# Kernel tuning notes

Measured on AMD Instinct MI355X. Metric: run time of the kernel, lower is better.

The kernel has to match this reference:

```python
import jax, jax.numpy as jnp
import numpy as np

B, S, IN = 16, 512, 32
D, H, L = 768, 12, 6
DH = D // H
DFF = 4 * D
EPS = 1e-5
NEG = -1e9


def _ln(x, g, b):
    m = jnp.mean(x, axis=-1, keepdims=True)
    v = jnp.mean(jnp.square(x - m), axis=-1, keepdims=True)
    return (x - m) * jax.lax.rsqrt(v + EPS) * g + b


def setup_inputs() -> dict:
    key = jax.random.key(0)
    ks = jax.random.split(key, 24)
    nrm = lambda k, shape, s=0.02: jax.random.normal(k, shape, jnp.float32) * s
    inp = {
        'x': jax.random.normal(ks[0], (B, S, IN), jnp.float32),
        'event_lengths': jax.random.randint(ks[1], (B,), 1, S + 1),
        'in_w': nrm(ks[2], (IN, D)),
        'in_b': jnp.zeros((D,), jnp.float32),
        'pos_emb': nrm(ks[3], (S, D)),
        'qw': nrm(ks[4], (L, D, D)), 'qb': jnp.zeros((L, D), jnp.float32),
        'kw': nrm(ks[5], (L, D, D)), 'kb': jnp.zeros((L, D), jnp.float32),
        'vw': nrm(ks[6], (L, D, D)), 'vb': jnp.zeros((L, D), jnp.float32),
        'w1': nrm(ks[7], (L, D, DFF)), 'b1': jnp.zeros((L, DFF), jnp.float32),
        'w2': nrm(ks[8], (L, DFF, D)), 'b2': jnp.zeros((L, D), jnp.float32),
        'ln1_g': jnp.ones((L, D), jnp.float32), 'ln1_b': jnp.zeros((L, D), jnp.float32),
        'ln2_g': jnp.ones((L, D), jnp.float32), 'ln2_b': jnp.zeros((L, D), jnp.float32),
        'out_w': nrm(ks[9], (D, 1)), 'out_b': jnp.zeros((1,), jnp.float32),
    }
    return inp


def reference(x, event_lengths, in_w, in_b, pos_emb, qw, qb, kw, kb, vw, vb,
              w1, b1, w2, b2, ln1_g, ln1_b, ln2_g, ln2_b, out_w, out_b):
    b, s, _ = x.shape
    h = x @ in_w + in_b + pos_emb[None, :s]  # [B,S,D]
    valid = jnp.arange(s)[None, :] < event_lengths[:, None]  # [B,S]
    amask = valid[:, None, :, None] & valid[:, None, None, :]  # [B,1,S,S]
    scale = np.float32(1.0 / np.sqrt(DH))
    for l in range(qw.shape[0]):
        q = (h @ qw[l] + qb[l]).reshape(b, s, H, DH)
        k = (h @ kw[l] + kb[l]).reshape(b, s, H, DH)
        v = (h @ vw[l] + vb[l]).reshape(b, s, H, DH)
        scores = jnp.einsum('bqhd,bkhd->bhqk', q, k) * scale
        scores = jnp.where(amask, scores, NEG)
        p = jax.nn.softmax(scores, axis=-1)
        o = jnp.einsum('bhqk,bkhd->bqhd', p, v).reshape(b, s, -1)
        # NOTE: source overwrites summarize(...) output with the raw concat, so no out-proj
        h = _ln(h + o, ln1_g[l], ln1_b[l])
        ff = jnp.maximum(h @ w1[l] + b1[l], 0.0) @ w2[l] + b2[l]
        h = _ln(h + ff, ln2_g[l], ln2_b[l])
    pooled = jnp.where(valid[..., None], h, 0.0).sum(axis=1) / event_lengths[:, None].astype(h.dtype)
    return pooled @ out_w + out_b  # [B,1]
```

## Files before the change

### kernel.cpp

```cpp
#include <hip/hip_runtime.h>

typedef unsigned short u16;
typedef unsigned int u32;
typedef u16 u16x8 __attribute__((ext_vector_type(8)));
typedef u16 u16x4 __attribute__((ext_vector_type(4)));
typedef __bf16 bf16x8 __attribute__((ext_vector_type(8)));
typedef float f32x4 __attribute__((ext_vector_type(4)));

#define DEV __device__ __forceinline__

DEV u16 f2bf(float f) {
  u32 u = __builtin_bit_cast(u32, f);
  u32 r = u + 0x7fffu + ((u >> 16) & 1u);
  return (u16)(r >> 16);
}

DEV float bf2f(u16 v) { return __builtin_bit_cast(float, (u32)v << 16); }

DEV int imin(int a, int b) { return a < b ? a : b; }

DEV void gload_lds16(const void* g, void* l) {
  __builtin_amdgcn_global_load_lds(
      (const __attribute__((address_space(1))) void*)g,
      (__attribute__((address_space(3))) void*)l, 16, 0, 0);
}

template <int RELU, int VMODE, int PIPE>
__global__ __launch_bounds__(256, PIPE ? 2 : 3) void gemm97_kernel(
    const u16* __restrict__ A, const u16* __restrict__ Bt, const float* __restrict__ bias,
    u16* __restrict__ Cb, u16* __restrict__ vT, const int* __restrict__ lens, int M, int N, int K,
    int ldc) {
  __shared__ __align__(16) u16 As[(PIPE ? 2 : 1) * 128 * 64];
  __shared__ __align__(16) u16 Bs[(PIPE ? 2 : 1) * 128 * 64];
  const int t = threadIdx.x, wave = t >> 6, lane = t & 63;
  const int fr = lane & 15, fq = lane >> 4;
  const int NT = K >> 6;
  const int nbx = N >> 7;

  int bid = blockIdx.x;
  {
    const int cpx = (int)gridDim.x >> 3;
    bid = (bid & 7) * cpx + (bid >> 3);
  }
  const int bx = bid % nbx, by = bid / nbx;
  const int m0 = by << 7, n0 = bx << 7;
  if ((m0 & 511) >= lens[m0 >> 9]) return;

  const int srow = t >> 3;
  const int c8 = ((t & 7) ^ (srow & 7)) * 8;
  const u16* ag = A + (size_t)(m0 + srow) * K + c8;
  const u16* bg = Bt + (size_t)(n0 + srow) * K + c8;

  auto STAGE = [&](int buf, int kt) {
    char* a = (char*)As + buf * 16384 + wave * 1024;
    char* b = (char*)Bs + buf * 16384 + wave * 1024;
    const u16* agp = ag + (size_t)kt * 64;
    const u16* bgp = bg + (size_t)kt * 64;
#pragma unroll
    for (int i = 0; i < 4; ++i) {
      gload_lds16(agp + (size_t)i * 32 * K, a + i * 4096);
      gload_lds16(bgp + (size_t)i * 32 * K, b + i * 4096);
    }
  };

  const int wr = (wave >> 1) * 64, wc = (wave & 1) * 64;
  f32x4 acc[4][4] = {};

  if (PIPE) {
    STAGE(0, 0);
    asm volatile("s_waitcnt vmcnt(0)" ::: "memory");
    __syncthreads();
  }

  for (int kt = 0; kt < NT; ++kt) {
    const int cur = PIPE ? (kt & 1) : 0;
    if (PIPE) {
      if (kt + 1 < NT) STAGE(cur ^ 1, kt + 1);
    } else {
      STAGE(0, kt);
      asm volatile("s_waitcnt vmcnt(0)" ::: "memory");
      __syncthreads();
    }
    const u16* Ab = As + cur * 8192;
    const u16* Bb = Bs + cur * 8192;
#pragma unroll
    for (int ks = 0; ks < 2; ++ks) {
      bf16x8 af[4], bv[4];
#pragma unroll
      for (int m = 0; m < 4; ++m)
        af[m] = *(const bf16x8*)(Ab + (wr + m * 16 + fr) * 64 + (((ks * 4 + fq) ^ (fr & 7)) * 8));
#pragma unroll
      for (int n = 0; n < 4; ++n)
        bv[n] = *(const bf16x8*)(Bb + (wc + n * 16 + fr) * 64 + (((ks * 4 + fq) ^ (fr & 7)) * 8));
#pragma unroll
      for (int m = 0; m < 4; ++m)
#pragma unroll
        for (int n = 0; n < 4; ++n)
          acc[m][n] = __builtin_amdgcn_mfma_f32_16x16x32_bf16(af[m], bv[n], acc[m][n], 0, 0, 0);
    }
    if (PIPE) asm volatile("s_waitcnt vmcnt(0)" ::: "memory");
    __syncthreads();
  }

#pragma unroll
  for (int n = 0; n < 4; ++n) {
    const int colb = n0 + wc + n * 16;
    const int col = colb + fr;
    const float bvv = bias[col];
    if (VMODE && colb >= 1536) {
      const int dd = col - 1536;
      const int hh = dd >> 6, d6 = dd & 63;
#pragma unroll
      for (int m = 0; m < 4; ++m) {
        const int row0 = m0 + wr + m * 16 + fq * 4;
        const int bb = row0 >> 9, ss = row0 & 511;
        u16x4 pk;
#pragma unroll
        for (int r = 0; r < 4; ++r) pk[r] = f2bf(acc[m][n][r] + bvv);
        *(u16x4*)(vT + ((size_t)(bb * 12 + hh) * 64 + d6) * 512 + ss) = pk;
      }
    } else {
#pragma unroll
      for (int m = 0; m < 4; ++m) {
#pragma unroll
        for (int r = 0; r < 4; ++r) {
          const int row = m0 + wr + m * 16 + fq * 4 + r;
          float v = acc[m][n][r] + bvv;
          if (RELU) v = fmaxf(v, 0.f);
          Cb[(size_t)row * ldc + col] = f2bf(v);
        }
      }
    }
  }
}

__global__ __launch_bounds__(512) void attn_kernel(const u16* __restrict__ qk,
                                                   const u16* __restrict__ vT,
                                                   const int* __restrict__ lens,
                                                   u16* __restrict__ o) {
  __shared__ __align__(16) u16 Kl[128 * 64];
  __shared__ __align__(16) u16 Vt[64 * 128];
  __shared__ __align__(16) u16 Pl[8][16 * 128];

  const int bid = blockIdx.x;
  const int z = bid & 1;
  const int pair = bid >> 1;
  const int h = pair % 12;
  const int b = pair / 12;
  const int len = lens[b];
  if (z * 256 >= len) return;
  const int t = threadIdx.x, wave = t >> 6, lane = t & 63;
  const int fr = lane & 15, fq = lane >> 4;

  const size_t base = (size_t)b * 512 * 1536;
  const size_t vbase = (size_t)(b * 12 + h) * 64 * 512;
  const int q0w = z * 256 + wave * 32;

  bf16x8 qf[2][2];
#pragma unroll
  for (int qi = 0; qi < 2; ++qi)
#pragma unroll
    for (int ks = 0; ks < 2; ++ks)
      qf[qi][ks] = *(const bf16x8*)(qk + base + (size_t)(q0w + qi * 16 + fr) * 1536 + h * 64 +
                                    ks * 32 + fq * 8);

  f32x4 oacc[2][4] = {};
  float mrow[2][4], lrow[2][4];
#pragma unroll
  for (int qi = 0; qi < 2; ++qi)
#pragma unroll
    for (int r = 0; r < 4; ++r) {
      mrow[qi][r] = -1e30f;
      lrow[qi][r] = 0.f;
    }

  const int nt = (len + 127) >> 7;
  for (int kt = 0; kt < nt; ++kt) {
    const int kv0 = kt * 128;
#pragma unroll
    for (int i = 0; i < 2; ++i) {
      const int c = i * 512 + t;
      const int krow = c >> 3, kch = c & 7;
      u16x8 kvl = *(const u16x8*)(qk + base + (size_t)(kv0 + krow) * 1536 + 768 + h * 64 + kch * 8);
      *(u16x8*)(Kl + krow * 64 + ((kch ^ (krow & 7)) * 8)) = kvl;
      const int d = c >> 4, vch = c & 15;
      u16x8 vv = *(const u16x8*)(vT + vbase + (size_t)d * 512 + kv0 + vch * 8);
      *(u16x8*)(Vt + d * 128 + ((vch ^ (d & 7)) * 8)) = vv;
    }
    __syncthreads();

#pragma unroll
    for (int qi = 0; qi < 2; ++qi) {
      if (q0w + qi * 16 >= len) break;
      f32x4 sa[8] = {};
#pragma unroll
      for (int ks = 0; ks < 2; ++ks) {
#pragma unroll
        for (int n = 0; n < 8; ++n) {
          const int colr = n * 16 + fr;
          bf16x8 kf = *(const bf16x8*)(Kl + colr * 64 + (((ks * 4 + fq) ^ (colr & 7)) * 8));
          sa[n] = __builtin_amdgcn_mfma_f32_16x16x32_bf16(qf[qi][ks], kf, sa[n], 0, 0, 0);
        }
      }

      float tm[4] = {-1e30f, -1e30f, -1e30f, -1e30f};
#pragma unroll
      for (int n = 0; n < 8; ++n) {
        const int col = kv0 + n * 16 + fr;
        const bool ok = col < len;
#pragma unroll
        for (int r = 0; r < 4; ++r) {
          const float s = ok ? sa[n][r] * 0.125f : -1e30f;
          sa[n][r] = s;
          tm[r] = fmaxf(tm[r], s);
        }
      }
#pragma unroll
      for (int d = 1; d < 16; d <<= 1)
#pragma unroll
        for (int r = 0; r < 4; ++r) tm[r] = fmaxf(tm[r], __shfl_xor(tm[r], d));

      float al[4], rs[4];
#pragma unroll
      for (int r = 0; r < 4; ++r) {
        const float mn = fmaxf(mrow[qi][r], tm[r]);
        al[r] = __expf(mrow[qi][r] - mn);
        mrow[qi][r] = mn;
        rs[r] = 0.f;
      }
#pragma unroll
      for (int n = 0; n < 8; ++n)
#pragma unroll
        for (int r = 0; r < 4; ++r) {
          const float p = __expf(sa[n][r] - mrow[qi][r]);
          sa[n][r] = p;
          rs[r] += p;
        }
#pragma unroll
      for (int d = 1; d < 16; d <<= 1)
#pragma unroll
        for (int r = 0; r < 4; ++r) rs[r] += __shfl_xor(rs[r], d);
#pragma unroll
      for (int r = 0; r < 4; ++r) lrow[qi][r] = lrow[qi][r] * al[r] + rs[r];
#pragma unroll
      for (int n = 0; n < 4; ++n)
#pragma unroll
        for (int r = 0; r < 4; ++r) oacc[qi][n][r] *= al[r];

      u16* P = &Pl[wave][0];
#pragma unroll
      for (int n = 0; n < 8; ++n) {
        const int col = n * 16 + fr;
#pragma unroll
        for (int r = 0; r < 4; ++r) {
          const int row = fq * 4 + r;
          P[row * 128 + (((col >> 3) ^ (row & 7)) * 8) + (col & 7)] = f2bf(sa[n][r]);
        }
      }
#pragma unroll
      for (int kslot = 0; kslot < 4; ++kslot) {
        const int ch = kslot * 4 + fq;
        bf16x8 pa = *(const bf16x8*)(P + fr * 128 + ((ch ^ (fr & 7)) * 8));
#pragma unroll
        for (int n = 0; n < 4; ++n) {
          const int colv = n * 16 + fr;
          bf16x8 vf = *(const bf16x8*)(Vt + colv * 128 + ((ch ^ (colv & 7)) * 8));
          oacc[qi][n] = __builtin_amdgcn_mfma_f32_16x16x32_bf16(pa, vf, oacc[qi][n], 0, 0, 0);
        }
      }
    }
    __syncthreads();
  }

  const size_t obase = (size_t)b * 512 * 768 + (size_t)q0w * 768 + h * 64;
#pragma unroll
  for (int qi = 0; qi < 2; ++qi) {
    if (q0w + qi * 16 >= len) break;
#pragma unroll
    for (int n = 0; n < 4; ++n)
#pragma unroll
      for (int r = 0; r < 4; ++r)
        o[obase + (size_t)(qi * 16 + fq * 4 + r) * 768 + n * 16 + fr] =
            f2bf(oacc[qi][n][r] / lrow[qi][r]);
  }
}

__global__ __launch_bounds__(256) void transpose_all_kernel(
    const float* __restrict__ qw, const float* __restrict__ kw, const float* __restrict__ vw,
    const float* __restrict__ w1, const float* __restrict__ w2, u16* __restrict__ qkvt6,
    u16* __restrict__ w1t6, u16* __restrict__ w2t6) {
  __shared__ u16 tile[64 * 66];
  const int l = blockIdx.y;
  int x = blockIdx.x;
  const float* in;
  u16* op;
  int K, N, nbx;
  if (x < 432) {
    const int which = x / 144;
    x -= which * 144;
    in = (which == 0 ? qw : which == 1 ? kw : vw) + (size_t)l * 768 * 768;
    op = qkvt6 + (size_t)l * 2304 * 768 + (size_t)which * 768 * 768;
    K = 768;
    N = 768;
    nbx = 12;
  } else if (x < 1008) {
    x -= 432;
    in = w1 + (size_t)l * 768 * 3072;
    op = w1t6 + (size_t)l * 3072 * 768;
    K = 768;
    N = 3072;
    nbx = 48;
  } else {
    x -= 1008;
    in = w2 + (size_t)l * 3072 * 768;
    op = w2t6 + (size_t)l * 768 * 3072;
    K = 3072;
    N = 768;
    nbx = 12;
  }
  const int n0 = (x % nbx) * 64, k0 = (x / nbx) * 64;
  const int lr = threadIdx.x >> 4;
  const int lc = threadIdx.x & 15;
#pragma unroll
  for (int i = 0; i < 4; ++i) {
    const int kr = i * 16 + lr;
    f32x4 v = *(const f32x4*)(in + (size_t)(k0 + kr) * N + n0 + lc * 4);
#pragma unroll
    for (int j = 0; j < 4; ++j) tile[(lc * 4 + j) * 66 + kr] = f2bf(v[j]);
  }
  __syncthreads();
#pragma unroll
  for (int i = 0; i < 4; ++i) {
    const int nr = i * 16 + lr;
    u16x4 pk;
#pragma unroll
    for (int j = 0; j < 4; ++j) pk[j] = tile[nr * 66 + lc * 4 + j];
    *(u16x4*)(op + (size_t)(n0 + nr) * K + k0 + lc * 4) = pk;
  }
}

__global__ __launch_bounds__(256) void inproj_kernel(const float* __restrict__ x,
                                                     const float* __restrict__ in_w,
                                                     const float* __restrict__ in_b,
                                                     const float* __restrict__ pos,
                                                     float* __restrict__ h,
                                                     u16* __restrict__ hbf) {
  __shared__ float xs[8][32];
  const int t = threadIdx.x;
  const int row0 = blockIdx.x * 8;
  xs[t >> 5][t & 31] = x[(size_t)row0 * 32 + t];
  __syncthreads();
#pragma unroll
  for (int j = 0; j < 3; ++j) {
    const int d = t + j * 256;
    float acc[8] = {};
#pragma unroll
    for (int i = 0; i < 32; ++i) {
      const float wv = in_w[i * 768 + d];
#pragma unroll
      for (int r = 0; r < 8; ++r) acc[r] += xs[r][i] * wv;
    }
    const float bb = in_b[d];
#pragma unroll
    for (int r = 0; r < 8; ++r) {
      const int row = row0 + r;
      const int s = row & 511;
      const float v = acc[r] + bb + pos[(size_t)s * 768 + d];
      h[(size_t)row * 768 + d] = v;
      hbf[(size_t)row * 768 + d] = f2bf(v);
    }
  }
}

__global__ __launch_bounds__(256) void ln_kernel(const float* __restrict__ hin,
                                                 const u16* __restrict__ delta,
                                                 const int* __restrict__ lens,
                                                 const float* __restrict__ g,
                                                 const float* __restrict__ bb,
                                                 float* __restrict__ hout,
                                                 u16* __restrict__ hbf) {
  const int row = blockIdx.x * 4 + (threadIdx.x >> 6);
  if ((row & 511) >= lens[row >> 9]) return;
  const int lane = threadIdx.x & 63;
  const size_t rb = (size_t)row * 768 + lane * 4;
  f32x4 xv[3];
  float s = 0.f, s2 = 0.f;
#pragma unroll
  for (int j = 0; j < 3; ++j) {
    f32x4 a = *(const f32x4*)(hin + rb + j * 256);
    u16x4 dv = *(const u16x4*)(delta + rb + j * 256);
    f32x4 v;
#pragma unroll
    for (int c = 0; c < 4; ++c) v[c] = a[c] + bf2f(dv[c]);
    xv[j] = v;
    s += v[0] + v[1] + v[2] + v[3];
    s2 += v[0] * v[0] + v[1] * v[1] + v[2] * v[2] + v[3] * v[3];
  }
#pragma unroll
  for (int d = 1; d < 64; d <<= 1) {
    s += __shfl_xor(s, d);
    s2 += __shfl_xor(s2, d);
  }
  const float mean = s * (1.f / 768.f);
  const float var = fmaxf(s2 * (1.f / 768.f) - mean * mean, 0.f);
  const float rstd = rsqrtf(var + 1e-5f);
#pragma unroll
  for (int j = 0; j < 3; ++j) {
    f32x4 gv = *(const f32x4*)(g + lane * 4 + j * 256);
    f32x4 bv = *(const f32x4*)(bb + lane * 4 + j * 256);
    f32x4 y;
    u16x4 yb;
#pragma unroll
    for (int c = 0; c < 4; ++c) {
      y[c] = (xv[j][c] - mean) * rstd * gv[c] + bv[c];
      yb[c] = f2bf(y[c]);
    }
    *(f32x4*)(hout + rb + j * 256) = y;
    *(u16x4*)(hbf + rb + j * 256) = yb;
  }
}

__global__ __launch_bounds__(256) void pool1_kernel(const float* __restrict__ h,
                                                    const int* __restrict__ lens,
                                                    const float* __restrict__ ow,
                                                    float* __restrict__ wsp) {
  const int b = blockIdx.x >> 3, chunk = blockIdx.x & 7;
  const int len = lens[b];
  const int t = threadIdx.x;
  const int s0 = chunk * 64;
  const int s1 = imin(s0 + 64, len);
  float acc0 = 0.f, acc1 = 0.f, acc2 = 0.f;
  const float* hp = h + (size_t)b * 512 * 768;
  for (int s = s0; s < s1; ++s) {
    const size_t rb = (size_t)s * 768;
    acc0 += hp[rb + t];
    acc1 += hp[rb + t + 256];
    acc2 += hp[rb + t + 512];
  }
  float part = acc0 * ow[t] + acc1 * ow[t + 256] + acc2 * ow[t + 512];
#pragma unroll
  for (int d = 1; d < 64; d <<= 1) part += __shfl_xor(part, d);
  __shared__ float ps[4];
  if ((t & 63) == 0) ps[t >> 6] = part;
  __syncthreads();
  if (t == 0) wsp[blockIdx.x] = ps[0] + ps[1] + ps[2] + ps[3];
}

__global__ void pool2_kernel(const float* __restrict__ wsp, const int* __restrict__ lens,
                             const float* __restrict__ ob, float* __restrict__ out) {
  const int b = threadIdx.x;
  if (b < 16) {
    float s = 0.f;
#pragma unroll
    for (int c = 0; c < 8; ++c) s += wsp[b * 8 + c];
    out[b] = s / (float)lens[b] + ob[0];
  }
}

__global__ void biaspack_kernel(const float* __restrict__ qb, const float* __restrict__ kb,
                                const float* __restrict__ vb, float* __restrict__ qkvb) {
  const int i = blockIdx.x * 256 + threadIdx.x;
  if (i >= 6 * 2304) return;
  const int l = i / 2304, j = i % 2304;
  float v;
  if (j < 768)
    v = qb[l * 768 + j];
  else if (j < 1536)
    v = kb[l * 768 + j - 768];
  else
    v = vb[l * 768 + j - 1536];
  qkvb[i] = v;
}

extern "C" void kernel_launch(void* const* d_in, const int* in_sizes, int n_in, void* d_out,
                              int out_size, void* d_ws, size_t ws_size, hipStream_t stream) {
  const float* x = (const float*)d_in[0];
  const int* lens = (const int*)d_in[1];
  const float* in_w = (const float*)d_in[2];
  const float* in_b = (const float*)d_in[3];
  const float* pos = (const float*)d_in[4];
  const float* qw = (const float*)d_in[5];
  const float* qb = (const float*)d_in[6];
  const float* kw = (const float*)d_in[7];
  const float* kb = (const float*)d_in[8];
  const float* vw = (const float*)d_in[9];
  const float* vb = (const float*)d_in[10];
  const float* w1 = (const float*)d_in[11];
  const float* b1 = (const float*)d_in[12];
  const float* w2 = (const float*)d_in[13];
  const float* b2 = (const float*)d_in[14];
  const float* ln1g = (const float*)d_in[15];
  const float* ln1b = (const float*)d_in[16];
  const float* ln2g = (const float*)d_in[17];
  const float* ln2b = (const float*)d_in[18];
  const float* ow = (const float*)d_in[19];
  const float* ob = (const float*)d_in[20];
  float* out = (float*)d_out;

  char* w = (char*)d_ws;
  size_t off = 0;
  auto alloc = [&](size_t bytes) -> void* {
    void* p = w + off;
    off += (bytes + 255) & ~(size_t)255;
    return p;
  };
  u16* qkvt6 = (u16*)alloc((size_t)6 * 2304 * 768 * 2);
  u16* w1t6 = (u16*)alloc((size_t)6 * 3072 * 768 * 2);
  u16* w2t6 = (u16*)alloc((size_t)6 * 768 * 3072 * 2);
  float* qkvb = (float*)alloc((size_t)6 * 2304 * 4);
  float* h = (float*)alloc((size_t)8192 * 768 * 4);
  u16* hbf = (u16*)alloc((size_t)8192 * 768 * 2);
  u16* obuf = (u16*)alloc((size_t)8192 * 768 * 2);
  u16* ubuf = (u16*)alloc((size_t)8192 * 3072 * 2);
  float* wsp = (float*)alloc((size_t)128 * 4);
  u16* qkbuf = ubuf;
  u16* vT = ubuf + (size_t)8192 * 1536;
  u16* ffbuf = ubuf;

  biaspack_kernel<<<(6 * 2304 + 255) / 256, 256, 0, stream>>>(qb, kb, vb, qkvb);
  transpose_all_kernel<<<dim3(1584, 6), 256, 0, stream>>>(qw, kw, vw, w1, w2, qkvt6, w1t6, w2t6);
  inproj_kernel<<<1024, 256, 0, stream>>>(x, in_w, in_b, pos, h, hbf);

  for (int l = 0; l < 6; ++l) {
    gemm97_kernel<0, 1, 0><<<1152, 256, 0, stream>>>(hbf, qkvt6 + (size_t)l * 2304 * 768,
                                                     qkvb + l * 2304, qkbuf, vT, lens, 8192, 2304,
                                                     768, 1536);
    attn_kernel<<<384, 512, 0, stream>>>(qkbuf, vT, lens, obuf);
    ln_kernel<<<2048, 256, 0, stream>>>(h, obuf, lens, ln1g + l * 768, ln1b + l * 768, h, hbf);
    gemm97_kernel<1, 0, 1><<<1536, 256, 0, stream>>>(hbf, w1t6 + (size_t)l * 3072 * 768,
                                                     b1 + l * 3072, ffbuf, nullptr, lens, 8192,
                                                     3072, 768, 3072);
    gemm97_kernel<0, 0, 0><<<384, 256, 0, stream>>>(ffbuf, w2t6 + (size_t)l * 768 * 3072,
                                                    b2 + l * 768, obuf, nullptr, lens, 8192, 768,
                                                    3072, 768);
    ln_kernel<<<2048, 256, 0, stream>>>(h, obuf, lens, ln2g + l * 768, ln2b + l * 768, h, hbf);
  }
  pool1_kernel<<<128, 256, 0, stream>>>(h, lens, ow, wsp);
  pool2_kernel<<<1, 64, 0, stream>>>(wsp, lens, ob, out);
  (void)in_sizes;
  (void)n_in;
  (void)out_size;
  (void)ws_size;
}
```

Baseline: 1.324 ms.

## Always double-buffer GEMM tiles and simplify weight transpose kernel

Removes the PIPE template parameter so every GEMM (QKV, FFN1, FFN2) uses the double-buffered LDS staging path with launch bounds allowing two blocks per CU, instead of single-buffered staging at three blocks per CU for QKV and FFN2. The idea is to overlap global-to-LDS loads with MFMA work in all GEMMs, at the cost of doubled LDS use and lower occupancy for those two. Separately, the weight transpose kernel is rewritten to use scalar float loads into a padded fp32 tile and scalar bf16 stores, replacing 16-byte vector loads and 8-byte packed stores. This makes its memory accesses narrower.

New measurement: 1.358 ms. 1.03x slower.

```diff
diff --git a/kernel.cpp b/kernel.cpp
--- a/kernel.cpp
+++ b/kernel.cpp
@@ -25,13 +25,13 @@
       (__attribute__((address_space(3))) void*)l, 16, 0, 0);
 }
 
-template <int RELU, int VMODE, int PIPE>
-__global__ __launch_bounds__(256, PIPE ? 2 : 3) void gemm97_kernel(
+template <int RELU, int VMODE>
+__global__ __launch_bounds__(256, 2) void gemm97_kernel(
     const u16* __restrict__ A, const u16* __restrict__ Bt, const float* __restrict__ bias,
     u16* __restrict__ Cb, u16* __restrict__ vT, const int* __restrict__ lens, int M, int N, int K,
     int ldc) {
-  __shared__ __align__(16) u16 As[(PIPE ? 2 : 1) * 128 * 64];
-  __shared__ __align__(16) u16 Bs[(PIPE ? 2 : 1) * 128 * 64];
+  __shared__ __align__(16) u16 As[2 * 128 * 64];
+  __shared__ __align__(16) u16 Bs[2 * 128 * 64];
   const int t = threadIdx.x, wave = t >> 6, lane = t & 63;
   const int fr = lane & 15, fq = lane >> 4;
   const int NT = K >> 6;
@@ -66,21 +66,13 @@
   const int wr = (wave >> 1) * 64, wc = (wave & 1) * 64;
   f32x4 acc[4][4] = {};
 
-  if (PIPE) {
-    STAGE(0, 0);
-    asm volatile("s_waitcnt vmcnt(0)" ::: "memory");
-    __syncthreads();
-  }
+  STAGE(0, 0);
+  asm volatile("s_waitcnt vmcnt(0)" ::: "memory");
+  __syncthreads();
 
   for (int kt = 0; kt < NT; ++kt) {
-    const int cur = PIPE ? (kt & 1) : 0;
-    if (PIPE) {
-      if (kt + 1 < NT) STAGE(cur ^ 1, kt + 1);
-    } else {
-      STAGE(0, kt);
-      asm volatile("s_waitcnt vmcnt(0)" ::: "memory");
-      __syncthreads();
-    }
+    const int cur = kt & 1;
+    if (kt + 1 < NT) STAGE(cur ^ 1, kt + 1);
     const u16* Ab = As + cur * 8192;
     const u16* Bb = Bs + cur * 8192;
 #pragma unroll
@@ -98,7 +90,7 @@
         for (int n = 0; n < 4; ++n)
           acc[m][n] = __builtin_amdgcn_mfma_f32_16x16x32_bf16(af[m], bv[n], acc[m][n], 0, 0, 0);
     }
-    if (PIPE) asm volatile("s_waitcnt vmcnt(0)" ::: "memory");
+    asm volatile("s_waitcnt vmcnt(0)" ::: "memory");
     __syncthreads();
   }
 
@@ -289,7 +281,7 @@
     const float* __restrict__ qw, const float* __restrict__ kw, const float* __restrict__ vw,
     const float* __restrict__ w1, const float* __restrict__ w2, u16* __restrict__ qkvt6,
     u16* __restrict__ w1t6, u16* __restrict__ w2t6) {
-  __shared__ u16 tile[64 * 66];
+  __shared__ float tile[64][65];
   const int l = blockIdx.y;
   int x = blockIdx.x;
   const float* in;
@@ -318,25 +310,15 @@
     N = 768;
     nbx = 12;
   }
+  const int tx = threadIdx.x & 63, ty = threadIdx.x >> 6;
   const int n0 = (x % nbx) * 64, k0 = (x / nbx) * 64;
-  const int lr = threadIdx.x >> 4;
-  const int lc = threadIdx.x & 15;
-#pragma unroll
-  for (int i = 0; i < 4; ++i) {
-    const int kr = i * 16 + lr;
-    f32x4 v = *(const f32x4*)(in + (size_t)(k0 + kr) * N + n0 + lc * 4);
-#pragma unroll
-    for (int j = 0; j < 4; ++j) tile[(lc * 4 + j) * 66 + kr] = f2bf(v[j]);
-  }
+#pragma unroll
+  for (int i = 0; i < 16; ++i)
+    tile[ty + i * 4][tx] = in[(size_t)(k0 + ty + i * 4) * N + n0 + tx];
   __syncthreads();
 #pragma unroll
-  for (int i = 0; i < 4; ++i) {
-    const int nr = i * 16 + lr;
-    u16x4 pk;
-#pragma unroll
-    for (int j = 0; j < 4; ++j) pk[j] = tile[nr * 66 + lc * 4 + j];
-    *(u16x4*)(op + (size_t)(n0 + nr) * K + k0 + lc * 4) = pk;
-  }
+  for (int i = 0; i < 16; ++i)
+    op[(size_t)(n0 + ty + i * 4) * K + k0 + tx] = f2bf(tile[tx][ty + i * 4]);
 }
 
 __global__ __launch_bounds__(256) void inproj_kernel(const float* __restrict__ x,
@@ -522,17 +504,17 @@
   inproj_kernel<<<1024, 256, 0, stream>>>(x, in_w, in_b, pos, h, hbf);
 
   for (int l = 0; l < 6; ++l) {
-    gemm97_kernel<0, 1, 0><<<1152, 256, 0, stream>>>(hbf, qkvt6 + (size_t)l * 2304 * 768,
-                                                     qkvb + l * 2304, qkbuf, vT, lens, 8192, 2304,
-                                                     768, 1536);
+    gemm97_kernel<0, 1><<<1152, 256, 0, stream>>>(hbf, qkvt6 + (size_t)l * 2304 * 768,
+                                                  qkvb + l * 2304, qkbuf, vT, lens, 8192, 2304,
+                                                  768, 1536);
     attn_kernel<<<384, 512, 0, stream>>>(qkbuf, vT, lens, obuf);
     ln_kernel<<<2048, 256, 0, stream>>>(h, obuf, lens, ln1g + l * 768, ln1b + l * 768, h, hbf);
-    gemm97_kernel<1, 0, 1><<<1536, 256, 0, stream>>>(hbf, w1t6 + (size_t)l * 3072 * 768,
-                                                     b1 + l * 3072, ffbuf, nullptr, lens, 8192,
-                                                     3072, 768, 3072);
-    gemm97_kernel<0, 0, 0><<<384, 256, 0, stream>>>(ffbuf, w2t6 + (size_t)l * 768 * 3072,
-                                                    b2 + l * 768, obuf, nullptr, lens, 8192, 768,
-                                                    3072, 768);
+    gemm97_kernel<1, 0><<<1536, 256, 0, stream>>>(hbf, w1t6 + (size_t)l * 3072 * 768,
+                                                  b1 + l * 3072, ffbuf, nullptr, lens, 8192, 3072,
+                                                  768, 3072);
+    gemm97_kernel<0, 0><<<384, 256, 0, stream>>>(ffbuf, w2t6 + (size_t)l * 768 * 3072,
+                                                 b2 + l * 768, obuf, nullptr, lens, 8192, 768,
+                                                 3072, 768);
     ln_kernel<<<2048, 256, 0, stream>>>(h, obuf, lens, ln2g + l * 768, ln2b + l * 768, h, hbf);
   }
   pool1_kernel<<<128, 256, 0, stream>>>(h, lens, ow, wsp);
```
